# Kernel optimization log

Measured on AMD Instinct MI355X. Metric: run time of the kernel, lower is better.

## Reference

```python
import jax, jax.numpy as jnp
import numpy as np

N_NODES = 16384
N_EDGES = 196608
N_ELEM = 8
C = 32              # hidden channels per l-block
LMAX = 3
SH_DIM = 16         # (LMAX+1)^2
NUM_BESSEL = 8
R_MAX = 5.0
P_CUT = 5.0
H_RAD = 64
AVG_NEIGH = 12.0
N_LAYERS = 2
L_SLICES = ((0, 1), (1, 4), (4, 9), (9, 16))  # l = 0..3 blocks


def real_sph_harm(u):
    # u: [E,3] unit vectors -> real spherical harmonics up to l=3, component-normalized. [E,16]
    x, y, z = u[:, 0], u[:, 1], u[:, 2]
    x2, y2, z2 = x * x, y * y, z * z
    sh = [
        jnp.ones_like(x),
        jnp.sqrt(3.) * x, jnp.sqrt(3.) * y, jnp.sqrt(3.) * z,
        jnp.sqrt(15.) * x * y, jnp.sqrt(15.) * y * z,
        jnp.sqrt(5.) / 2. * (3. * z2 - 1.), jnp.sqrt(15.) * x * z,
        jnp.sqrt(15.) / 2. * (x2 - y2),
        jnp.sqrt(35. / 8.) * y * (3. * x2 - y2), jnp.sqrt(105.) * x * y * z,
        jnp.sqrt(21. / 8.) * y * (5. * z2 - 1.), jnp.sqrt(7.) / 2. * z * (5. * z2 - 3.),
        jnp.sqrt(21. / 8.) * x * (5. * z2 - 1.), jnp.sqrt(105.) / 2. * z * (x2 - y2),
        jnp.sqrt(35. / 8.) * x * (x2 - 3. * y2),
    ]
    return jnp.stack(sh, axis=-1)


def bessel_cutoff(r):
    # Bessel radial basis * polynomial cutoff (MACE radial embedding). r: [E] -> [E, NUM_BESSEL]
    u = r / R_MAX
    n = jnp.arange(1, NUM_BESSEL + 1, dtype=r.dtype)
    safe_r = jnp.maximum(r, 1e-9)
    rb = jnp.sqrt(2.0 / R_MAX) * jnp.sin(jnp.pi * n * u[:, None]) / safe_r[:, None]
    p = P_CUT
    fc = 1.0 - (p + 1.) * (p + 2.) / 2. * u ** p + p * (p + 2.) * u ** (p + 1.) - p * (p + 1.) / 2. * u ** (p + 2.)
    fc = fc * (u < 1.0).astype(r.dtype)
    return rb * fc[:, None]


def per_l_linear(a, W):
    # equivariant per-l channel mixing. a: [N,C,16], W: [4,C,C]
    outs = [jnp.einsum('nci,co->noi', a[:, :, s:e], W[l]) for l, (s, e) in enumerate(L_SLICES)]
    return jnp.concatenate(outs, axis=-1)


def mace_descriptors(atom_pos, node_attrs, shifts, edge_index,
                     W_embed, W1, W2, W3, W4, Wlin, Wskip, w2, w3, Wprod):
    snd, rcv = edge_index[0], edge_index[1]
    vec = atom_pos[rcv] - atom_pos[snd] + shifts            # [E,3]
    length = jnp.sqrt(jnp.sum(vec * vec, axis=-1) + 1e-18)  # [E]
    unit = vec / length[:, None]
    edge_attrs = real_sph_harm(unit)                        # [E,16]
    edge_feats = bessel_cutoff(length)                      # [E,8]

    node_scal = node_attrs @ W_embed                        # [N,C] node embedding (l=0)
    node_feats = jnp.zeros((atom_pos.shape[0], C, SH_DIM), dtype=atom_pos.dtype).at[:, :, 0].set(node_scal)

    descs = []
    for i in range(N_LAYERS):
        # radial MLP -> per-edge tensor-product weights
        h = jax.nn.silu(edge_feats @ W1[i])
        h = jax.nn.silu(h @ W2[i])
        h = jax.nn.silu(h @ W3[i])
        tpw = (h @ W4[i]).reshape(-1, C, SH_DIM)            # [E,C,16]
        # gather -> channelwise tensor product with edge spherical harmonics
        s = node_feats[:, :, 0][snd]                        # [E,C] invariant sender feats
        msg = tpw * edge_attrs[:, None, :] * s[:, :, None]  # [E,C,16]
        # scatter-add aggregation
        agg = jax.ops.segment_sum(msg.reshape(-1, C * SH_DIM), rcv,
                                  num_segments=N_NODES) / AVG_NEIGH
        a = per_l_linear(agg.reshape(-1, C, SH_DIM), Wlin[i])
        # element-dependent residual (skip tensor product with one-hot node attrs)
        sc = jnp.einsum('nz,ncm,zco->nom', node_attrs, node_feats, Wskip[i])
        # symmetric-contraction-style product block (correlation up to 3, invariants)
        inv = a[:, :, 0]
        p2 = jnp.sum(a * a, axis=-1)                        # power-spectrum invariant [N,C]
        b0 = inv + w2[i] * p2 + w3[i] * inv * p2
        b = a.at[:, :, 0].set(b0)
        node_feats = per_l_linear(b, Wprod[i]) + sc
        descs.append(node_feats[:, :, 0])                   # invariant slice
    return jnp.concatenate(descs, axis=-1)                  # [N, N_LAYERS*C]


def setup_inputs() -> dict:
    key = jax.random.key(0)
    ks = jax.random.split(key, 16)
    atom_pos = jax.random.normal(ks[0], (N_NODES, 3), dtype=jnp.float32) * 1.8
    elem = jax.random.randint(ks[1], (N_NODES,), 0, N_ELEM)
    node_attrs = jax.nn.one_hot(elem, N_ELEM, dtype=jnp.float32)
    shifts = jnp.zeros((N_EDGES, 3), dtype=jnp.float32)
    edge_index = jax.random.randint(ks[2], (2, N_EDGES), 0, N_NODES)
    f32 = jnp.float32
    W_embed = jax.random.normal(ks[3], (N_ELEM, C), f32) / np.sqrt(N_ELEM)
    W1 = jax.random.normal(ks[4], (N_LAYERS, NUM_BESSEL, H_RAD), f32) / np.sqrt(NUM_BESSEL)
    W2 = jax.random.normal(ks[5], (N_LAYERS, H_RAD, H_RAD), f32) / np.sqrt(H_RAD)
    W3 = jax.random.normal(ks[6], (N_LAYERS, H_RAD, H_RAD), f32) / np.sqrt(H_RAD)
    W4 = jax.random.normal(ks[7], (N_LAYERS, H_RAD, C * SH_DIM), f32) / np.sqrt(H_RAD)
    Wlin = jax.random.normal(ks[8], (N_LAYERS, 4, C, C), f32) / np.sqrt(C)
    Wskip = jax.random.normal(ks[9], (N_LAYERS, N_ELEM, C, C), f32) / np.sqrt(N_ELEM * C)
    w2 = jax.random.normal(ks[10], (N_LAYERS, C), f32) * 0.1
    w3 = jax.random.normal(ks[11], (N_LAYERS, C), f32) * 0.1
    Wprod = jax.random.normal(ks[12], (N_LAYERS, 4, C, C), f32) / np.sqrt(C)
    return {"atom_pos": atom_pos, "node_attrs": node_attrs, "shifts": shifts,
            "edge_index": edge_index, "W_embed": W_embed, "W1": W1, "W2": W2,
            "W3": W3, "W4": W4, "Wlin": Wlin, "Wskip": Wskip, "w2": w2,
            "w3": w3, "Wprod": Wprod}


def reference(atom_pos, node_attrs, shifts, edge_index, W_embed, W1, W2, W3, W4,
              Wlin, Wskip, w2, w3, Wprod):
    return mace_descriptors(atom_pos, node_attrs, shifts, edge_index,
                            W_embed, W1, W2, W3, W4, Wlin, Wskip, w2, w3, Wprod)
```

## Files before the change

### kernel.cpp

```cpp
#include <hip/hip_runtime.h>
#include <math.h>

#define N_NODES_C 16384
#define N_EDGES_C 196608

typedef short bf16x8 __attribute__((ext_vector_type(8)));
typedef float f32x4 __attribute__((ext_vector_type(4)));
typedef float f32x8 __attribute__((ext_vector_type(8)));

__device__ __forceinline__ float silu_f(float x) {
  return x * __builtin_amdgcn_rcpf(1.0f + __expf(-x));
}

__global__ void k_count(const int* __restrict__ rcv, int* __restrict__ counts) {
  int e = blockIdx.x * 256 + threadIdx.x;
  atomicAdd(&counts[rcv[e]], 1);
}

__global__ __launch_bounds__(1024) void k_scan(const int* __restrict__ counts,
                                               int* __restrict__ row_start,
                                               int* __restrict__ cursor) {
  __shared__ int sums[1024];
  const int tid = threadIdx.x;
  int loc[16];
  int s = 0;
#pragma unroll
  for (int i = 0; i < 16; ++i) { loc[i] = counts[tid * 16 + i]; s += loc[i]; }
  sums[tid] = s;
  __syncthreads();
  for (int off = 1; off < 1024; off <<= 1) {
    int t = (tid >= off) ? sums[tid - off] : 0;
    __syncthreads();
    sums[tid] += t;
    __syncthreads();
  }
  int excl = sums[tid] - s;
#pragma unroll
  for (int i = 0; i < 16; ++i) {
    row_start[tid * 16 + i] = excl;
    cursor[tid * 16 + i] = excl;
    excl += loc[i];
  }
  if (tid == 1023) row_start[N_NODES_C] = excl;
}

__global__ void k_fill(const int* __restrict__ rcv, int* __restrict__ cursor,
                       int* __restrict__ elist) {
  int e = blockIdx.x * 256 + threadIdx.x;
  int slot = atomicAdd(&cursor[rcv[e]], 1);
  elist[slot] = e;
}

__global__ void k_elem(const float* __restrict__ attrs, int* __restrict__ elem) {
  int n = blockIdx.x * 256 + threadIdx.x;
  const float* a = attrs + n * 8;
  int best = 0;
  float bv = a[0];
#pragma unroll
  for (int z = 1; z < 8; ++z) {
    if (a[z] > bv) { bv = a[z]; best = z; }
  }
  elem[n] = best;
}

__global__ void k_embed(const float* __restrict__ attrs, const float* __restrict__ Wemb,
                        float* __restrict__ scal0, float* __restrict__ nf) {
  int gid = blockIdx.x * 256 + threadIdx.x;
  int n = gid >> 5, c = gid & 31;
  float s = 0.f;
#pragma unroll
  for (int z = 0; z < 8; ++z) s = fmaf(attrs[n * 8 + z], Wemb[z * 32 + c], s);
  scal0[gid] = s;
  float* row = nf + (size_t)n * 512 + c * 16;
  *(float4*)&row[0] = make_float4(s, 0.f, 0.f, 0.f);
  *(float4*)&row[4] = make_float4(0.f, 0.f, 0.f, 0.f);
  *(float4*)&row[8] = make_float4(0.f, 0.f, 0.f, 0.f);
  *(float4*)&row[12] = make_float4(0.f, 0.f, 0.f, 0.f);
}

__global__ __launch_bounds__(256, 3) void k_radial(
    const float* __restrict__ pos, const float* __restrict__ shifts,
    const int* __restrict__ snd, const int* __restrict__ rcv,
    const int* __restrict__ elist, const float* __restrict__ scal,
    const float* __restrict__ W1g, const float* __restrict__ W2g,
    const float* __restrict__ W3g, unsigned short* __restrict__ h3,
    float* __restrict__ sedge, float* __restrict__ Yout, const int writeY) {
  __shared__ __align__(16) float efs[4][32][8];
  __shared__ __align__(16) float hbs[4][64];
  const int wid = threadIdx.x >> 6, lane = threadIdx.x & 63;
  float w1c[8], w2c[64], w3c[64];
#pragma unroll
  for (int k = 0; k < 8; ++k) w1c[k] = W1g[k * 64 + lane];
#pragma unroll
  for (int k = 0; k < 64; ++k) w2c[k] = W2g[k * 64 + lane];
#pragma unroll
  for (int k = 0; k < 64; ++k) w3c[k] = W3g[k * 64 + lane];

  const int base = (blockIdx.x * 4 + wid) * 32;

  if (lane < 32) {
    const int p = base + lane;
    const int e = elist[p];
    const int sn = snd[e], rc = rcv[e];
    const float vx = pos[rc * 3 + 0] - pos[sn * 3 + 0] + shifts[e * 3 + 0];
    const float vy = pos[rc * 3 + 1] - pos[sn * 3 + 1] + shifts[e * 3 + 1];
    const float vz = pos[rc * 3 + 2] - pos[sn * 3 + 2] + shifts[e * 3 + 2];
    const float len = __builtin_amdgcn_sqrtf(vx * vx + vy * vy + vz * vz + 1e-18f);
    const float u = len * 0.2f;
    float fc = 0.f;
    if (u < 1.0f) {
      const float u2 = u * u, u5 = u2 * u2 * u;
      fc = 1.0f - 21.0f * u5 + 35.0f * u5 * u - 15.0f * u5 * u2;
    }
    const float pref = 0.6324555320336759f * fc * __builtin_amdgcn_rcpf(fmaxf(len, 1e-9f));
    float efv[8];
#pragma unroll
    for (int k = 0; k < 8; ++k) {
      const float pin = 3.14159274f * (float)(k + 1);
      efv[k] = pref * __sinf(pin * u);
    }
    *(float4*)&efs[wid][lane][0] = make_float4(efv[0], efv[1], efv[2], efv[3]);
    *(float4*)&efs[wid][lane][4] = make_float4(efv[4], efv[5], efv[6], efv[7]);

    if (writeY) {
      const float il = __builtin_amdgcn_rcpf(len);
      const float x = vx * il, y = vy * il, z = vz * il;
      const float x2 = x * x, y2 = y * y, z2 = z * z;
      const float s3 = 1.7320508075688772f;
      const float s15 = 3.872983346207417f;
      const float s5h = 1.118033988749895f;
      const float s35_8 = 2.091650066335189f;
      const float s105 = 10.246950765959598f;
      const float s21_8 = 1.6201851746019651f;
      const float s7h = 1.3228756555322954f;
      const float s105h = 5.123475382979799f;
      float* yp = Yout + (size_t)p * 16;
      *(float4*)&yp[0] = make_float4(1.f, s3 * x, s3 * y, s3 * z);
      *(float4*)&yp[4] = make_float4(s15 * x * y, s15 * y * z, s5h * (3.f * z2 - 1.f), s15 * x * z);
      *(float4*)&yp[8] = make_float4(0.5f * s15 * (x2 - y2), s35_8 * y * (3.f * x2 - y2),
                                     s105 * x * y * z, s21_8 * y * (5.f * z2 - 1.f));
      *(float4*)&yp[12] = make_float4(s7h * z * (5.f * z2 - 3.f), s21_8 * x * (5.f * z2 - 1.f),
                                      s105h * z * (x2 - y2), s35_8 * x * (x2 - 3.f * y2));
    }
  }

  {
    const int p2 = base + (lane >> 1);
    const int e2 = elist[p2];
    const int sn2 = snd[e2];
    const int co = (lane & 1) * 16;
    const float* sp = scal + (size_t)sn2 * 32 + co;
    float* dp = sedge + (size_t)p2 * 32 + co;
    *(float4*)&dp[0] = *(const float4*)&sp[0];
    *(float4*)&dp[4] = *(const float4*)&sp[4];
    *(float4*)&dp[8] = *(const float4*)&sp[8];
    *(float4*)&dp[12] = *(const float4*)&sp[12];
  }

  for (int t = 0; t < 32; ++t) {
    const float4 ef0 = *(const float4*)&efs[wid][t][0];
    const float4 ef1 = *(const float4*)&efs[wid][t][4];
    float a1 = ef0.x * w1c[0];
    a1 = fmaf(ef0.y, w1c[1], a1);
    a1 = fmaf(ef0.z, w1c[2], a1);
    a1 = fmaf(ef0.w, w1c[3], a1);
    a1 = fmaf(ef1.x, w1c[4], a1);
    a1 = fmaf(ef1.y, w1c[5], a1);
    a1 = fmaf(ef1.z, w1c[6], a1);
    a1 = fmaf(ef1.w, w1c[7], a1);
    hbs[wid][lane] = silu_f(a1);
    float p0 = 0.f, p1 = 0.f, p2 = 0.f, p3 = 0.f;
#pragma unroll
    for (int k4 = 0; k4 < 16; ++k4) {
      const float4 hb = *(const float4*)&hbs[wid][k4 * 4];
      p0 = fmaf(hb.x, w2c[k4 * 4 + 0], p0);
      p1 = fmaf(hb.y, w2c[k4 * 4 + 1], p1);
      p2 = fmaf(hb.z, w2c[k4 * 4 + 2], p2);
      p3 = fmaf(hb.w, w2c[k4 * 4 + 3], p3);
    }
    hbs[wid][lane] = silu_f((p0 + p1) + (p2 + p3));
    p0 = p1 = p2 = p3 = 0.f;
#pragma unroll
    for (int k4 = 0; k4 < 16; ++k4) {
      const float4 hb = *(const float4*)&hbs[wid][k4 * 4];
      p0 = fmaf(hb.x, w3c[k4 * 4 + 0], p0);
      p1 = fmaf(hb.y, w3c[k4 * 4 + 1], p1);
      p2 = fmaf(hb.z, w3c[k4 * 4 + 2], p2);
      p3 = fmaf(hb.w, w3c[k4 * 4 + 3], p3);
    }
    const float hv = silu_f((p0 + p1) + (p2 + p3));
    const unsigned hb16 = __float_as_uint(hv) & 0xFFFF0000u;
    const float lof = hv - __uint_as_float(hb16);
    h3[(size_t)(base + t) * 128 + lane] = (unsigned short)(hb16 >> 16);
    h3[(size_t)(base + t) * 128 + 64 + lane] = (unsigned short)(__float_as_uint(lof) >> 16);
  }
}

__global__ __launch_bounds__(256, 3) void k_gather(
    const unsigned short* __restrict__ h3, const float* __restrict__ W4g,
    const float* __restrict__ Yb, const float* __restrict__ sedge,
    const int* __restrict__ row_start, float* __restrict__ agg) {
  const int ch = (blockIdx.x >> 3) & 1;
  const int ng = ((blockIdx.x >> 4) << 3) | (blockIdx.x & 7);
  const int w = threadIdx.x >> 6, lane = threadIdx.x & 63;
  const int grp = lane >> 4, lm = lane & 15;

  bf16x8 bhi[4][2], blo[4][2];
#pragma unroll
  for (int t = 0; t < 4; ++t) {
    const int col = ch * 256 + w * 64 + t * 16 + lm;
#pragma unroll
    for (int kk = 0; kk < 2; ++kk) {
#pragma unroll
      for (int j = 0; j < 8; ++j) {
        const float wv = W4g[(kk * 32 + grp * 8 + j) * 512 + col];
        const unsigned hb = __float_as_uint(wv) & 0xFFFF0000u;
        bhi[t][kk][j] = (short)(hb >> 16);
        blo[t][kk][j] = (short)(__float_as_uint(wv - __uint_as_float(hb)) >> 16);
      }
    }
  }

  const int nBeg = ng * 16;
  for (int n = nBeg; n < nBeg + 16; ++n) {
    const int e0 = row_start[n], e1 = row_start[n + 1];
    float outv[4] = {0.f, 0.f, 0.f, 0.f};
    for (int p0 = e0; p0 < e1; p0 += 16) {
      bf16x8 ahi0 = {0, 0, 0, 0, 0, 0, 0, 0}, ahi1 = ahi0, alo0 = ahi0, alo1 = ahi0;
      const int pa = p0 + lm;
      if (pa < e1) {
        const unsigned short* hp = h3 + (size_t)pa * 128 + grp * 8;
        ahi0 = *(const bf16x8*)(hp);
        ahi1 = *(const bf16x8*)(hp + 32);
        alo0 = *(const bf16x8*)(hp + 64);
        alo1 = *(const bf16x8*)(hp + 96);
      }
      const f32x8 sv = *(const f32x8*)(sedge + (size_t)p0 * 32 + lane * 8);
      float Yv[4];
#pragma unroll
      for (int r = 0; r < 4; ++r)
        Yv[r] = Yb[(size_t)(p0 + grp * 4 + r) * 16 + lm];
#pragma unroll
      for (int t = 0; t < 4; ++t) {
        f32x4 acc = {0.f, 0.f, 0.f, 0.f};
        acc = __builtin_amdgcn_mfma_f32_16x16x32_bf16(ahi0, bhi[t][0], acc, 0, 0, 0);
        acc = __builtin_amdgcn_mfma_f32_16x16x32_bf16(ahi1, bhi[t][1], acc, 0, 0, 0);
        acc = __builtin_amdgcn_mfma_f32_16x16x32_bf16(alo0, bhi[t][0], acc, 0, 0, 0);
        acc = __builtin_amdgcn_mfma_f32_16x16x32_bf16(alo1, bhi[t][1], acc, 0, 0, 0);
        acc = __builtin_amdgcn_mfma_f32_16x16x32_bf16(ahi0, blo[t][0], acc, 0, 0, 0);
        acc = __builtin_amdgcn_mfma_f32_16x16x32_bf16(ahi1, blo[t][1], acc, 0, 0, 0);
        float cp = 0.f;
#pragma unroll
        for (int r = 0; r < 4; ++r) {
          const float srt = __shfl(sv[(w & 1) * 4 + t], ((grp * 4 + r) << 2) | (ch * 2) | (w >> 1));
          cp = fmaf(acc[r] * Yv[r], srt, cp);
        }
        outv[t] += cp;
      }
    }
    const float inv12 = 1.0f / 12.0f;
#pragma unroll
    for (int t = 0; t < 4; ++t) {
      outv[t] += __shfl_xor(outv[t], 16);
      outv[t] += __shfl_xor(outv[t], 32);
      if (grp == t)
        agg[(size_t)n * 512 + ch * 256 + w * 64 + t * 16 + lm] = outv[t] * inv12;
    }
  }
}

__global__ __launch_bounds__(256) void k_node(
    const float* __restrict__ agg, float* __restrict__ nf,
    const float* __restrict__ Wlin, const float* __restrict__ Wprod,
    const float* __restrict__ Wskip, const float* __restrict__ w2v,
    const float* __restrict__ w3v, const int* __restrict__ elem,
    float* __restrict__ scal_out, float* __restrict__ dout, const int layer) {
  __shared__ __align__(16) float aggs[8][512];
  __shared__ __align__(16) float nfs[8][512];
  __shared__ float bs[8][544];
  const int tid = threadIdx.x;
  const int n0 = blockIdx.x * 8;
  for (int i = tid; i < 1024; i += 256) {
    const int nl = i >> 7, qq = i & 127;
    ((f32x4*)aggs)[i] = ((const f32x4*)agg)[(size_t)(n0 + nl) * 128 + qq];
    ((f32x4*)nfs)[i] = ((const f32x4*)nf)[(size_t)(n0 + nl) * 128 + qq];
  }
  __syncthreads();
  const int nl = tid >> 5, o = tid & 31;
  const int n = n0 + nl;
  constexpr int SLa[4] = {0, 1, 4, 9};
  constexpr int ELa[4] = {1, 4, 9, 16};
  float a[16];
#pragma unroll
  for (int m = 0; m < 16; ++m) a[m] = 0.f;
#pragma unroll
  for (int l = 0; l < 4; ++l) {
    for (int c = 0; c < 32; ++c) {
      const float w = Wlin[(l * 32 + c) * 32 + o];
#pragma unroll
      for (int m = SLa[l]; m < ELa[l]; ++m) a[m] = fmaf(aggs[nl][c * 16 + m], w, a[m]);
    }
  }
  const float inv = a[0];
  float p2 = 0.f;
#pragma unroll
  for (int m = 0; m < 16; ++m) p2 = fmaf(a[m], a[m], p2);
  a[0] = inv + w2v[o] * p2 + w3v[o] * inv * p2;
#pragma unroll
  for (int m = 0; m < 16; ++m) bs[nl][o * 17 + m] = a[m];
  __syncthreads();
  float outv[16];
#pragma unroll
  for (int m = 0; m < 16; ++m) outv[m] = 0.f;
#pragma unroll
  for (int l = 0; l < 4; ++l) {
    for (int c = 0; c < 32; ++c) {
      const float w = Wprod[(l * 32 + c) * 32 + o];
#pragma unroll
      for (int m = SLa[l]; m < ELa[l]; ++m) outv[m] = fmaf(bs[nl][c * 17 + m], w, outv[m]);
    }
  }
  const int z = elem[n];
  const float* wsk = Wskip + z * 1024;
  for (int c = 0; c < 32; ++c) {
    const float w = wsk[c * 32 + o];
#pragma unroll
    for (int m = 0; m < 16; ++m) outv[m] = fmaf(nfs[nl][c * 16 + m], w, outv[m]);
  }
  float* op = nf + (size_t)n * 512 + o * 16;
  *(float4*)&op[0] = make_float4(outv[0], outv[1], outv[2], outv[3]);
  *(float4*)&op[4] = make_float4(outv[4], outv[5], outv[6], outv[7]);
  *(float4*)&op[8] = make_float4(outv[8], outv[9], outv[10], outv[11]);
  *(float4*)&op[12] = make_float4(outv[12], outv[13], outv[14], outv[15]);
  scal_out[n * 32 + o] = outv[0];
  dout[(size_t)n * 64 + layer * 32 + o] = outv[0];
}

extern "C" void kernel_launch(void* const* d_in, const int* in_sizes, int n_in,
                              void* d_out, int out_size, void* d_ws, size_t ws_size,
                              hipStream_t stream) {
  const float* pos = (const float*)d_in[0];
  const float* attrs = (const float*)d_in[1];
  const float* shifts = (const float*)d_in[2];
  const int* eidx = (const int*)d_in[3];
  const float* W_embed = (const float*)d_in[4];
  const float* W1 = (const float*)d_in[5];
  const float* W2 = (const float*)d_in[6];
  const float* W3 = (const float*)d_in[7];
  const float* W4 = (const float*)d_in[8];
  const float* Wlin = (const float*)d_in[9];
  const float* Wskip = (const float*)d_in[10];
  const float* w2v = (const float*)d_in[11];
  const float* w3v = (const float*)d_in[12];
  const float* Wprod = (const float*)d_in[13];
  float* out = (float*)d_out;
  const int* snd = eidx;
  const int* rcv = eidx + N_EDGES_C;

  char* p = (char*)d_ws;
  auto take = [&](size_t bytes) {
    char* q = p;
    p += (bytes + 255) & ~(size_t)255;
    return q;
  };
  int* counts = (int*)take((size_t)N_NODES_C * 4);
  int* row_start = (int*)take((size_t)(N_NODES_C + 1) * 4);
  int* cursor = (int*)take((size_t)N_NODES_C * 4);
  int* elist = (int*)take((size_t)N_EDGES_C * 4);
  int* elem = (int*)take((size_t)N_NODES_C * 4);
  float* Ybuf = (float*)take((size_t)(N_EDGES_C + 16) * 16 * 4);
  unsigned short* h3 = (unsigned short*)take((size_t)(N_EDGES_C + 16) * 128 * 2);
  float* sedge = (float*)take((size_t)(N_EDGES_C + 16) * 32 * 4);
  float* agg = (float*)take((size_t)N_NODES_C * 512 * 4);
  float* nf = (float*)take((size_t)N_NODES_C * 512 * 4);
  float* scal0 = (float*)take((size_t)N_NODES_C * 32 * 4);
  float* scal1 = (float*)take((size_t)N_NODES_C * 32 * 4);
  (void)ws_size; (void)in_sizes; (void)n_in; (void)out_size;

  hipMemsetAsync(counts, 0, (size_t)N_NODES_C * 4, stream);
  k_count<<<N_EDGES_C / 256, 256, 0, stream>>>(rcv, counts);
  k_scan<<<1, 1024, 0, stream>>>(counts, row_start, cursor);
  k_fill<<<N_EDGES_C / 256, 256, 0, stream>>>(rcv, cursor, elist);
  k_elem<<<N_NODES_C / 256, 256, 0, stream>>>(attrs, elem);
  k_embed<<<N_NODES_C * 32 / 256, 256, 0, stream>>>(attrs, W_embed, scal0, nf);

  for (int i = 0; i < 2; ++i) {
    k_radial<<<1536, 256, 0, stream>>>(pos, shifts, snd, rcv, elist,
                                       i == 0 ? scal0 : scal1,
                                       W1 + (size_t)i * 8 * 64, W2 + (size_t)i * 64 * 64,
                                       W3 + (size_t)i * 64 * 64, h3, sedge, Ybuf,
                                       i == 0 ? 1 : 0);
    k_gather<<<2048, 256, 0, stream>>>(h3, W4 + (size_t)i * 64 * 512, Ybuf, sedge,
                                       row_start, agg);
    k_node<<<N_NODES_C / 8, 256, 0, stream>>>(agg, nf, Wlin + (size_t)i * 4096,
                                              Wprod + (size_t)i * 4096,
                                              Wskip + (size_t)i * 8192,
                                              w2v + (size_t)i * 32, w3v + (size_t)i * 32,
                                              elem, scal1, out, i);
  }
}
```

Measured before the change: 512.6 us.

## Process two edges per radial MLP step and move W4 low bf16 part to LDS

The radial MLP now handles two edges per loop iteration, sharing the register-resident weights and overlapping two independent dependency chains. In the gather kernel, the low bf16 half of the split W4 weights moves from registers to LDS to cut VGPR pressure, and launch bounds rise to 4 waves per SIMD. The gather grid doubles with 8 nodes per block instead of 16. The shuffle-based sedge broadcast is replaced by direct float4 loads premultiplied with Y. This trades extra LDS traffic and redundant global loads for higher occupancy and ILP.

Result: slower. 535.8 us (+4.5%).

```diff
diff --git a/kernel.cpp b/kernel.cpp
--- a/kernel.cpp
+++ b/kernel.cpp
@@ -86,7 +86,7 @@
     const float* __restrict__ W3g, unsigned short* __restrict__ h3,
     float* __restrict__ sedge, float* __restrict__ Yout, const int writeY) {
   __shared__ __align__(16) float efs[4][32][8];
-  __shared__ __align__(16) float hbs[4][64];
+  __shared__ __align__(16) float hbs[4][2][64];
   const int wid = threadIdx.x >> 6, lane = threadIdx.x & 63;
   float w1c[8], w2c[64], w3c[64];
 #pragma unroll
@@ -157,72 +157,89 @@
     *(float4*)&dp[12] = *(const float4*)&sp[12];
   }
 
-  for (int t = 0; t < 32; ++t) {
-    const float4 ef0 = *(const float4*)&efs[wid][t][0];
-    const float4 ef1 = *(const float4*)&efs[wid][t][4];
-    float a1 = ef0.x * w1c[0];
-    a1 = fmaf(ef0.y, w1c[1], a1);
-    a1 = fmaf(ef0.z, w1c[2], a1);
-    a1 = fmaf(ef0.w, w1c[3], a1);
-    a1 = fmaf(ef1.x, w1c[4], a1);
-    a1 = fmaf(ef1.y, w1c[5], a1);
-    a1 = fmaf(ef1.z, w1c[6], a1);
-    a1 = fmaf(ef1.w, w1c[7], a1);
-    hbs[wid][lane] = silu_f(a1);
-    float p0 = 0.f, p1 = 0.f, p2 = 0.f, p3 = 0.f;
+  for (int t = 0; t < 16; ++t) {
+    const float4 eA0 = *(const float4*)&efs[wid][t][0];
+    const float4 eA1 = *(const float4*)&efs[wid][t][4];
+    const float4 eB0 = *(const float4*)&efs[wid][t + 16][0];
+    const float4 eB1 = *(const float4*)&efs[wid][t + 16][4];
+    float aA = eA0.x * w1c[0], aB = eB0.x * w1c[0];
+    aA = fmaf(eA0.y, w1c[1], aA); aB = fmaf(eB0.y, w1c[1], aB);
+    aA = fmaf(eA0.z, w1c[2], aA); aB = fmaf(eB0.z, w1c[2], aB);
+    aA = fmaf(eA0.w, w1c[3], aA); aB = fmaf(eB0.w, w1c[3], aB);
+    aA = fmaf(eA1.x, w1c[4], aA); aB = fmaf(eB1.x, w1c[4], aB);
+    aA = fmaf(eA1.y, w1c[5], aA); aB = fmaf(eB1.y, w1c[5], aB);
+    aA = fmaf(eA1.z, w1c[6], aA); aB = fmaf(eB1.z, w1c[6], aB);
+    aA = fmaf(eA1.w, w1c[7], aA); aB = fmaf(eB1.w, w1c[7], aB);
+    hbs[wid][0][lane] = silu_f(aA);
+    hbs[wid][1][lane] = silu_f(aB);
+    float pA0 = 0.f, pA1 = 0.f, pA2 = 0.f, pA3 = 0.f;
+    float pB0 = 0.f, pB1 = 0.f, pB2 = 0.f, pB3 = 0.f;
 #pragma unroll
     for (int k4 = 0; k4 < 16; ++k4) {
-      const float4 hb = *(const float4*)&hbs[wid][k4 * 4];
-      p0 = fmaf(hb.x, w2c[k4 * 4 + 0], p0);
-      p1 = fmaf(hb.y, w2c[k4 * 4 + 1], p1);
-      p2 = fmaf(hb.z, w2c[k4 * 4 + 2], p2);
-      p3 = fmaf(hb.w, w2c[k4 * 4 + 3], p3);
-    }
-    hbs[wid][lane] = silu_f((p0 + p1) + (p2 + p3));
-    p0 = p1 = p2 = p3 = 0.f;
+      const float4 hA = *(const float4*)&hbs[wid][0][k4 * 4];
+      const float4 hB = *(const float4*)&hbs[wid][1][k4 * 4];
+      pA0 = fmaf(hA.x, w2c[k4 * 4 + 0], pA0); pB0 = fmaf(hB.x, w2c[k4 * 4 + 0], pB0);
+      pA1 = fmaf(hA.y, w2c[k4 * 4 + 1], pA1); pB1 = fmaf(hB.y, w2c[k4 * 4 + 1], pB1);
+      pA2 = fmaf(hA.z, w2c[k4 * 4 + 2], pA2); pB2 = fmaf(hB.z, w2c[k4 * 4 + 2], pB2);
+      pA3 = fmaf(hA.w, w2c[k4 * 4 + 3], pA3); pB3 = fmaf(hB.w, w2c[k4 * 4 + 3], pB3);
+    }
+    hbs[wid][0][lane] = silu_f((pA0 + pA1) + (pA2 + pA3));
+    hbs[wid][1][lane] = silu_f((pB0 + pB1) + (pB2 + pB3));
+    pA0 = pA1 = pA2 = pA3 = 0.f;
+    pB0 = pB1 = pB2 = pB3 = 0.f;
 #pragma unroll
     for (int k4 = 0; k4 < 16; ++k4) {
-      const float4 hb = *(const float4*)&hbs[wid][k4 * 4];
-      p0 = fmaf(hb.x, w3c[k4 * 4 + 0], p0);
-      p1 = fmaf(hb.y, w3c[k4 * 4 + 1], p1);
-      p2 = fmaf(hb.z, w3c[k4 * 4 + 2], p2);
-      p3 = fmaf(hb.w, w3c[k4 * 4 + 3], p3);
-    }
-    const float hv = silu_f((p0 + p1) + (p2 + p3));
-    const unsigned hb16 = __float_as_uint(hv) & 0xFFFF0000u;
-    const float lof = hv - __uint_as_float(hb16);
-    h3[(size_t)(base + t) * 128 + lane] = (unsigned short)(hb16 >> 16);
-    h3[(size_t)(base + t) * 128 + 64 + lane] = (unsigned short)(__float_as_uint(lof) >> 16);
-  }
-}
-
-__global__ __launch_bounds__(256, 3) void k_gather(
+      const float4 hA = *(const float4*)&hbs[wid][0][k4 * 4];
+      const float4 hB = *(const float4*)&hbs[wid][1][k4 * 4];
+      pA0 = fmaf(hA.x, w3c[k4 * 4 + 0], pA0); pB0 = fmaf(hB.x, w3c[k4 * 4 + 0], pB0);
+      pA1 = fmaf(hA.y, w3c[k4 * 4 + 1], pA1); pB1 = fmaf(hB.y, w3c[k4 * 4 + 1], pB1);
+      pA2 = fmaf(hA.z, w3c[k4 * 4 + 2], pA2); pB2 = fmaf(hB.z, w3c[k4 * 4 + 2], pB2);
+      pA3 = fmaf(hA.w, w3c[k4 * 4 + 3], pA3); pB3 = fmaf(hB.w, w3c[k4 * 4 + 3], pB3);
+    }
+    const float hvA = silu_f((pA0 + pA1) + (pA2 + pA3));
+    const float hvB = silu_f((pB0 + pB1) + (pB2 + pB3));
+    const unsigned hbA = __float_as_uint(hvA) & 0xFFFF0000u;
+    const unsigned hbB = __float_as_uint(hvB) & 0xFFFF0000u;
+    const float loA = hvA - __uint_as_float(hbA);
+    const float loB = hvB - __uint_as_float(hbB);
+    h3[(size_t)(base + t) * 128 + lane] = (unsigned short)(hbA >> 16);
+    h3[(size_t)(base + t) * 128 + 64 + lane] = (unsigned short)(__float_as_uint(loA) >> 16);
+    h3[(size_t)(base + 16 + t) * 128 + lane] = (unsigned short)(hbB >> 16);
+    h3[(size_t)(base + 16 + t) * 128 + 64 + lane] = (unsigned short)(__float_as_uint(loB) >> 16);
+  }
+}
+
+__global__ __launch_bounds__(256, 4) void k_gather(
     const unsigned short* __restrict__ h3, const float* __restrict__ W4g,
     const float* __restrict__ Yb, const float* __restrict__ sedge,
     const int* __restrict__ row_start, float* __restrict__ agg) {
+  __shared__ __align__(16) short blo_lds[4][4][2][64][8];
   const int ch = (blockIdx.x >> 3) & 1;
   const int ng = ((blockIdx.x >> 4) << 3) | (blockIdx.x & 7);
   const int w = threadIdx.x >> 6, lane = threadIdx.x & 63;
   const int grp = lane >> 4, lm = lane & 15;
 
-  bf16x8 bhi[4][2], blo[4][2];
+  bf16x8 bhi[4][2];
 #pragma unroll
   for (int t = 0; t < 4; ++t) {
     const int col = ch * 256 + w * 64 + t * 16 + lm;
 #pragma unroll
     for (int kk = 0; kk < 2; ++kk) {
+      bf16x8 lo;
 #pragma unroll
       for (int j = 0; j < 8; ++j) {
         const float wv = W4g[(kk * 32 + grp * 8 + j) * 512 + col];
         const unsigned hb = __float_as_uint(wv) & 0xFFFF0000u;
         bhi[t][kk][j] = (short)(hb >> 16);
-        blo[t][kk][j] = (short)(__float_as_uint(wv - __uint_as_float(hb)) >> 16);
+        lo[j] = (short)(__float_as_uint(wv - __uint_as_float(hb)) >> 16);
       }
-    }
-  }
-
-  const int nBeg = ng * 16;
-  for (int n = nBeg; n < nBeg + 16; ++n) {
+      *(bf16x8*)&blo_lds[w][t][kk][lane][0] = lo;
+    }
+  }
+  __syncthreads();
+
+  const int nBeg = ng * 8;
+  for (int n = nBeg; n < nBeg + 8; ++n) {
     const int e0 = row_start[n], e1 = row_start[n + 1];
     float outv[4] = {0.f, 0.f, 0.f, 0.f};
     for (int p0 = e0; p0 < e1; p0 += 16) {
@@ -235,11 +252,17 @@
         alo0 = *(const bf16x8*)(hp + 64);
         alo1 = *(const bf16x8*)(hp + 96);
       }
-      const f32x8 sv = *(const f32x8*)(sedge + (size_t)p0 * 32 + lane * 8);
-      float Yv[4];
-#pragma unroll
-      for (int r = 0; r < 4; ++r)
-        Yv[r] = Yb[(size_t)(p0 + grp * 4 + r) * 16 + lm];
+      float ys[4][4];
+#pragma unroll
+      for (int r = 0; r < 4; ++r) {
+        const int pr = p0 + grp * 4 + r;
+        const float Yv = Yb[(size_t)pr * 16 + lm];
+        const float4 s4 = *(const float4*)&sedge[(size_t)pr * 32 + ch * 16 + w * 4];
+        ys[r][0] = Yv * s4.x;
+        ys[r][1] = Yv * s4.y;
+        ys[r][2] = Yv * s4.z;
+        ys[r][3] = Yv * s4.w;
+      }
 #pragma unroll
       for (int t = 0; t < 4; ++t) {
         f32x4 acc = {0.f, 0.f, 0.f, 0.f};
@@ -247,14 +270,14 @@
         acc = __builtin_amdgcn_mfma_f32_16x16x32_bf16(ahi1, bhi[t][1], acc, 0, 0, 0);
         acc = __builtin_amdgcn_mfma_f32_16x16x32_bf16(alo0, bhi[t][0], acc, 0, 0, 0);
         acc = __builtin_amdgcn_mfma_f32_16x16x32_bf16(alo1, bhi[t][1], acc, 0, 0, 0);
-        acc = __builtin_amdgcn_mfma_f32_16x16x32_bf16(ahi0, blo[t][0], acc, 0, 0, 0);
-        acc = __builtin_amdgcn_mfma_f32_16x16x32_bf16(ahi1, blo[t][1], acc, 0, 0, 0);
-        float cp = 0.f;
-#pragma unroll
-        for (int r = 0; r < 4; ++r) {
-          const float srt = __shfl(sv[(w & 1) * 4 + t], ((grp * 4 + r) << 2) | (ch * 2) | (w >> 1));
-          cp = fmaf(acc[r] * Yv[r], srt, cp);
-        }
+        const bf16x8 bl0 = *(const bf16x8*)&blo_lds[w][t][0][lane][0];
+        const bf16x8 bl1 = *(const bf16x8*)&blo_lds[w][t][1][lane][0];
+        acc = __builtin_amdgcn_mfma_f32_16x16x32_bf16(ahi0, bl0, acc, 0, 0, 0);
+        acc = __builtin_amdgcn_mfma_f32_16x16x32_bf16(ahi1, bl1, acc, 0, 0, 0);
+        float cp = acc[0] * ys[0][t];
+        cp = fmaf(acc[1], ys[1][t], cp);
+        cp = fmaf(acc[2], ys[2][t], cp);
+        cp = fmaf(acc[3], ys[3][t], cp);
         outv[t] += cp;
       }
     }
@@ -390,7 +413,7 @@
                                        W1 + (size_t)i * 8 * 64, W2 + (size_t)i * 64 * 64,
                                        W3 + (size_t)i * 64 * 64, h3, sedge, Ybuf,
                                        i == 0 ? 1 : 0);
-    k_gather<<<2048, 256, 0, stream>>>(h3, W4 + (size_t)i * 64 * 512, Ybuf, sedge,
+    k_gather<<<4096, 256, 0, stream>>>(h3, W4 + (size_t)i * 64 * 512, Ybuf, sedge,
                                        row_start, agg);
     k_node<<<N_NODES_C / 8, 256, 0, stream>>>(agg, nf, Wlin + (size_t)i * 4096,
                                               Wprod + (size_t)i * 4096,
```
